# Kernel optimization log

Measured on AMD Instinct MI355X. Metric: run time of the kernel, lower is better.

Reference implementation:

```python
import jax, jax.numpy as jnp
import numpy as np

D_MODEL = 2048
HQ = 32          # query heads
HKV = 8          # kv heads
HD = D_MODEL // HQ   # head_dim = 64
G = HQ // HKV        # group size = 4
THETA = 10000.0


def _rope(x, pos):
    """x: (B, H, T, D), pos: (B, T) int. Rotates even/odd interleaved pairs."""
    D = x.shape[-1]
    inv_freq = THETA ** (-jnp.arange(0, D, 2, dtype=jnp.float32) / D)   # (D/2,)
    ang = pos[:, None, :, None].astype(jnp.float32) * inv_freq          # (B,1,T,D/2)
    cos, sin = jnp.cos(ang), jnp.sin(ang)
    x1, x2 = x[..., 0::2], x[..., 1::2]
    r1 = x1 * cos - x2 * sin
    r2 = x1 * sin + x2 * cos
    return jnp.stack([r1, r2], axis=-1).reshape(x.shape)


def setup_inputs() -> dict:
    key = jax.random.key(0)
    ks = jax.random.split(key, 5)
    B, T = 2, 2048
    s = lambda fan_in: 1.0 / np.sqrt(fan_in)
    return {
        "x": jax.random.normal(ks[0], (B, T, D_MODEL), jnp.float32),
        "token_positions": jnp.arange(T, dtype=jnp.int32),
        "WQ": jax.random.normal(ks[1], (HQ * HD, D_MODEL), jnp.float32) * s(D_MODEL),
        "WK": jax.random.normal(ks[2], (HKV * HD, D_MODEL), jnp.float32) * s(D_MODEL),
        "WV": jax.random.normal(ks[3], (HKV * HD, D_MODEL), jnp.float32) * s(D_MODEL),
        "WO": jax.random.normal(ks[4], (D_MODEL, HQ * HD), jnp.float32) * s(HQ * HD),
    }


def reference(x, token_positions, WQ, WK, WV, WO):
    B, T, _ = x.shape
    pos = token_positions if token_positions.ndim == 2 else jnp.broadcast_to(token_positions[None, :], (B, T))

    # Projections (Linear is y = x @ W.T, no bias)
    Q = (x @ WQ.T).reshape(B, T, HQ, HD).transpose(0, 2, 1, 3)    # (B,Hq,T,D)
    K = (x @ WK.T).reshape(B, T, HKV, HD).transpose(0, 2, 1, 3)   # (B,Hkv,T,D)
    V = (x @ WV.T).reshape(B, T, HKV, HD).transpose(0, 2, 1, 3)

    Q = _rope(Q, pos)
    K = _rope(K, pos)

    # GQA: group query heads per kv head instead of duplicating K/V
    Qg = Q.reshape(B, HKV, G, T, HD)
    scale = jnp.float32(1.0 / np.sqrt(HD))
    scores = jnp.einsum('bkgqd,bkld->bkgql', Qg, K) * scale       # (B,Hkv,G,T,T)

    causal = jnp.tril(jnp.ones((T, T), dtype=bool))
    scores = jnp.where(causal, scores, jnp.finfo(scores.dtype).min)
    A = jax.nn.softmax(scores, axis=-1)

    O = jnp.einsum('bkgql,bkld->bkgqd', A, V)                     # (B,Hkv,G,T,D)
    O = O.reshape(B, HQ, T, HD).transpose(0, 2, 1, 3).reshape(B, T, HQ * HD)
    return O @ WO.T
```

## Files before the change

### kernel.cpp

```cpp
#include <hip/hip_runtime.h>
#include <hip/hip_bf16.h>

#define B_   2
#define T_   2048
#define DM_  2048
#define HQ_  32
#define HKV_ 8
#define HD_  64

typedef __attribute__((ext_vector_type(8))) short bf16x8;
typedef __attribute__((ext_vector_type(4))) float f32x4;
typedef __fp16 f16x4 __attribute__((ext_vector_type(4)));
typedef __fp16 f16x2 __attribute__((ext_vector_type(2)));

__device__ __forceinline__ unsigned short f2bf(float f) {
    unsigned int u = __float_as_uint(f);
    u = (u + 0x7fffu + ((u >> 16) & 1u)) >> 16;
    return (unsigned short)u;
}

__device__ __forceinline__ void gload16(const unsigned short* g, unsigned short* l) {
    __builtin_amdgcn_global_load_lds(
        (const __attribute__((address_space(1))) unsigned int*)g,
        (__attribute__((address_space(3))) unsigned int*)l, 16, 0, 0);
}


#define CONV_N 4718592

__global__ __launch_bounds__(256) void convert_all(
    const float* __restrict__ x,  const float* __restrict__ WQ,
    const float* __restrict__ WK, const float* __restrict__ WV,
    const float* __restrict__ WO, unsigned short* __restrict__ ws,
    const int* __restrict__ pos,  float* __restrict__ trig)
{
    int i = blockIdx.x*256 + threadIdx.x;
    if (i >= CONV_N) {
        int j = i - CONV_N;
        if (j < T_*32) {
            int t = j >> 5, p = j & 31;
            float inv = exp2f(-0.4152410118609203f * (float)p);
            float ang = (float)pos[t] * inv;
            float sn, cs;
            sincosf(ang, &sn, &cs);
            *(float2*)&trig[j*2] = make_float2(cs, sn);
        }
        return;
    }
    const float* src; unsigned short* dst; int rel;
    if (i < 2097152)      { src = x;  dst = ws;                 rel = i; }
    else if (i < 3145728) { src = WQ; dst = ws + 8388608;       rel = i - 2097152; }
    else if (i < 3407872) { src = WK; dst = ws + 8388608+4194304; rel = i - 3145728; }
    else if (i < 3670016) { src = WV; dst = ws + 8388608+5242880; rel = i - 3407872; }
    else                  { src = WO; dst = ws + 14680064;      rel = i - 3670016; }
    float4 v = *(const float4*)(src + (size_t)rel*4);
    uint2 pk;
    pk.x = (unsigned int)f2bf(v.x) | ((unsigned int)f2bf(v.y) << 16);
    pk.y = (unsigned int)f2bf(v.z) | ((unsigned int)f2bf(v.w) << 16);
    *(uint2*)(dst + (size_t)rel*4) = pk;
}

__global__ __launch_bounds__(256) void qkv_gemm_bf16(
    const unsigned short* __restrict__ Ab, const unsigned short* __restrict__ Wb,
    unsigned short* __restrict__ Qb, unsigned short* __restrict__ Kb,
    unsigned short* __restrict__ Vt, const float* __restrict__ trig)
{
    __shared__ unsigned short As[3][128*32];
    __shared__ unsigned short Bs[3][128*32];
    const int tid  = threadIdx.x;
    const int ln   = tid & 63;
    const int wv   = tid >> 6;
    const int wm   = (wv >> 1) * 64;
    const int wn   = (wv & 1) * 64;
    const int col  = ln & 15;
    const int quad = ln >> 4;

    const int bid = blockIdx.x;
    const int swz = (bid & 7) * 96 + (bid >> 3);
    const int n0  = (swz % 24) * 128;
    const int m0  = (swz / 24) * 128;

    const int cg = ((tid & 3) ^ ((tid >> 3) & 3)) * 8;
    const unsigned short* aG = Ab + (size_t)(m0 + (tid>>2))*DM_ + cg;
    const unsigned short* bG = Wb + (size_t)(n0 + (tid>>2))*DM_ + cg;
    const int ck = (quad ^ ((col >> 1) & 3)) * 8;

    f32x4 acc[4][4];
    #pragma unroll
    for (int i=0;i<4;++i)
        #pragma unroll
        for (int j=0;j<4;++j) { acc[i][j][0]=0.f; acc[i][j][1]=0.f; acc[i][j][2]=0.f; acc[i][j][3]=0.f; }

    auto stage = [&](int buf, int k0) {
        unsigned short* aL = &As[buf][wv*512];
        unsigned short* bL = &Bs[buf][wv*512];
        gload16(aG + k0,                  aL);
        gload16(aG + (size_t)64*DM_ + k0, aL + 2048);
        gload16(bG + k0,                  bL);
        gload16(bG + (size_t)64*DM_ + k0, bL + 2048);
    };

    auto kstep = [&](int bc, int k0v, int bstage, bool dostage, bool last) {
        if (last) asm volatile("s_waitcnt vmcnt(0)" ::: "memory");
        else      asm volatile("s_waitcnt vmcnt(4)" ::: "memory");
        __builtin_amdgcn_s_barrier();
        if (dostage) stage(bstage, k0v + 64);
        const unsigned short* Ac = As[bc];
        const unsigned short* Bc = Bs[bc];
        bf16x8 af[4], bfr[4];
        #pragma unroll
        for (int i2=0;i2<4;++i2) {
            af[i2]  = *(const bf16x8*)&Ac[(wm + i2*16 + col)*32 + ck];
            bfr[i2] = *(const bf16x8*)&Bc[(wn + i2*16 + col)*32 + ck];
        }
        #pragma unroll
        for (int i2=0;i2<4;++i2)
            #pragma unroll
            for (int j2=0;j2<4;++j2)
                acc[i2][j2] = __builtin_amdgcn_mfma_f32_16x16x32_bf16(af[i2], bfr[j2], acc[i2][j2], 0, 0, 0);
    };

    stage(0, 0);
    stage(1, 32);

    int k0 = 0;
    for (int rep = 0; rep < 20; ++rep) {
        kstep(0, k0,      2, true, false);
        kstep(1, k0+32,   0, true, false);
        kstep(2, k0+64,   1, true, false);
        k0 += 96;
    }
    kstep(0, 1920, 2, true,  false);
    kstep(1, 1952, 0, true,  false);
    kstep(2, 1984, 1, false, false);
    kstep(0, 2016, 0, false, true);

    const int b  = m0 >> 11;
    const int tb = m0 & 2047;
    #pragma unroll
    for (int j=0;j<4;++j) {
        const int n = n0 + wn + j*16 + col;
        if (n < 2560) {
            const int d   = n & 63;
            const int p   = d >> 1;
            const bool ev = (d & 1) == 0;
            const float sc = (n < 2048) ? 0.18033688011112042f : 1.0f;
            unsigned short* outp = (n < 2048)
                ? Qb + (((size_t)(b*HQ_  + (n>>6)))*T_)*HD_
                : Kb + (((size_t)(b*HKV_ + ((n-2048)>>6)))*T_)*HD_;
            #pragma unroll
            for (int i=0;i<4;++i) {
                const int t0 = tb + wm + i*16 + quad*4;
                #pragma unroll
                for (int r=0;r<4;++r) {
                    float self = acc[i][j][r];
                    float part = __shfl_xor(self, 1);
                    float2 cs  = *(const float2*)&trig[((t0 + r)*32 + p)*2];
                    float out  = ev ? (self*cs.x - part*cs.y)
                                    : (part*cs.y + self*cs.x);
                    out *= sc;
                    unsigned int pk = (unsigned int)f2bf(out);
                    unsigned int po = __shfl_xor(pk, 1);
                    if (ev)
                        *(unsigned int*)(outp + (size_t)(t0 + r)*HD_ + d) = pk | (po << 16);
                }
            }
        } else {
            #pragma unroll
            for (int i=0;i<4;++i) {
                const int t = tb + wm + i*16 + quad*4;
                unsigned short* vp = Vt + (((size_t)(b*HKV_ + ((n-2560)>>6)))*HD_ + (n&63))*T_ + t;
                union { f16x2 h; unsigned int u; } c0, c1;
                c0.h = __builtin_amdgcn_cvt_pkrtz(acc[i][j][0], acc[i][j][1]);
                c1.h = __builtin_amdgcn_cvt_pkrtz(acc[i][j][2], acc[i][j][3]);
                *(unsigned int*)(vp)     = c0.u;
                *(unsigned int*)(vp + 2) = c1.u;
            }
        }
    }
}

__global__ __launch_bounds__(256, 2) void attn_mfma(
    const unsigned short* __restrict__ Qb, const unsigned short* __restrict__ Kb,
    const unsigned short* __restrict__ Vh, unsigned short* __restrict__ Ob)
{
    __shared__ unsigned short Ks[2][64*64];
    __shared__ unsigned short Vs[2][64*64];

    const int tid  = threadIdx.x;
    const int lane = tid & 63;
    const int wave = tid >> 6;
    const int q16  = lane & 15;
    const int quad = lane >> 4;
    const int bxi  = blockIdx.x;
    const int bh   = blockIdx.y;
    const int b    = bh >> 5;
    const int h    = bh & 31;
    const int kvh  = h >> 2;
    const int qa   = bxi;
    const int qbt  = 31 - bxi;
    const int qgA  = qa *64 + wave*16 + q16;
    const int qgB  = qbt*64 + wave*16 + q16;

    const unsigned short* kbase = Kb + ((size_t)(b*HKV_ + kvh))*T_*HD_;
    const unsigned short* vbase = Vh + ((size_t)(b*HKV_ + kvh))*(size_t)HD_*T_;

    const bf16x8 qA0 = *(const bf16x8*)(Qb + ((size_t)bh*T_ + qgA)*HD_ + quad*8);
    const bf16x8 qA1 = *(const bf16x8*)(Qb + ((size_t)bh*T_ + qgA)*HD_ + 32 + quad*8);
    const bf16x8 qB0 = *(const bf16x8*)(Qb + ((size_t)bh*T_ + qgB)*HD_ + quad*8);
    const bf16x8 qB1 = *(const bf16x8*)(Qb + ((size_t)bh*T_ + qgB)*HD_ + 32 + quad*8);

    f32x4 oA[4], oB[4];
    #pragma unroll
    for (int i=0;i<4;++i) {
        oA[i][0]=0.f; oA[i][1]=0.f; oA[i][2]=0.f; oA[i][3]=0.f;
        oB[i][0]=0.f; oB[i][1]=0.f; oB[i][2]=0.f; oB[i][3]=0.f;
    }
    float lA = 0.f, lB = 0.f;

    const int sr = tid >> 3;
    const int sj = tid & 7;
    const int sc = (sj ^ (sr & 7)) * 8;

    const int rk7 = q16 & 7;
    const int ck0 = (quad ^ rk7) * 8;
    const int ck1 = ((quad + 4) ^ rk7) * 8;

    auto smrow = [&](const f32x4 s, float& ps) -> f16x4 {
        float e0 = exp2f(s[0]), e1 = exp2f(s[1]);
        float e2 = exp2f(s[2]), e3 = exp2f(s[3]);
        ps += (e0+e1) + (e2+e3);
        union { f16x2 h[2]; f16x4 v; } c;
        c.h[0] = __builtin_amdgcn_cvt_pkrtz(e0, e1);
        c.h[1] = __builtin_amdgcn_cvt_pkrtz(e2, e3);
        return c.v;
    };

    uint4 kr0, kr1, vr0, vr1;
    kr0 = *(const uint4*)(kbase + (size_t)sr*HD_ + sj*8);
    kr1 = *(const uint4*)(kbase + (size_t)(sr+32)*HD_ + sj*8);
    vr0 = *(const uint4*)(vbase + (size_t)sr*T_ + sj*8);
    vr1 = *(const uint4*)(vbase + (size_t)(sr+32)*T_ + sj*8);
    *(uint4*)&Ks[0][sr*64 + sc]      = kr0;
    *(uint4*)&Ks[0][(sr+32)*64 + sc] = kr1;
    *(uint4*)&Vs[0][sr*64 + sc]      = vr0;
    *(uint4*)&Vs[0][(sr+32)*64 + sc] = vr1;
    kr0 = *(const uint4*)(kbase + (size_t)(64+sr)*HD_ + sj*8);
    kr1 = *(const uint4*)(kbase + (size_t)(64+sr+32)*HD_ + sj*8);
    vr0 = *(const uint4*)(vbase + (size_t)sr*T_ + 64 + sj*8);
    vr1 = *(const uint4*)(vbase + (size_t)(sr+32)*T_ + 64 + sj*8);
    __syncthreads();

    int cur = 0;

    for (int kt = 0; kt <= qa; ++kt) {
        const unsigned short* KsC = Ks[cur];
        const unsigned short* VsC = Vs[cur];
        const int nxt = cur ^ 1;

        f32x4 sB[4], sA[4];
        #pragma unroll
        for (int t=0;t<4;++t) {
            sB[t][0]=0.f; sB[t][1]=0.f; sB[t][2]=0.f; sB[t][3]=0.f;
            sA[t][0]=0.f; sA[t][1]=0.f; sA[t][2]=0.f; sA[t][3]=0.f;
        }
        f16x4 pfB[4];
        float psB = 0.f, psA = 0.f;

        __builtin_amdgcn_s_setprio(1);
        #pragma unroll
        for (int t = 0; t < 4; ++t) {
            const int rk = (t*16 + q16) * 64;
            bf16x8 a0 = *(const bf16x8*)&KsC[rk + ck0];
            bf16x8 a1 = *(const bf16x8*)&KsC[rk + ck1];
            sB[t] = __builtin_amdgcn_mfma_f32_16x16x32_bf16(a0, qB0, sB[t], 0, 0, 0);
            sB[t] = __builtin_amdgcn_mfma_f32_16x16x32_bf16(a1, qB1, sB[t], 0, 0, 0);
            sA[t] = __builtin_amdgcn_mfma_f32_16x16x32_bf16(a0, qA0, sA[t], 0, 0, 0);
            sA[t] = __builtin_amdgcn_mfma_f32_16x16x32_bf16(a1, qA1, sA[t], 0, 0, 0);
            if (t > 0) pfB[t-1] = smrow(sB[t-1], psB);
        }
        *(uint4*)&Ks[nxt][sr*64 + sc]      = kr0;
        *(uint4*)&Ks[nxt][(sr+32)*64 + sc] = kr1;
        *(uint4*)&Vs[nxt][sr*64 + sc]      = vr0;
        *(uint4*)&Vs[nxt][(sr+32)*64 + sc] = vr1;
        if (kt + 1 < qbt) {
            const int kn = (kt+2)*64;
            kr0 = *(const uint4*)(kbase + (size_t)(kn+sr)*HD_ + sj*8);
            kr1 = *(const uint4*)(kbase + (size_t)(kn+sr+32)*HD_ + sj*8);
            vr0 = *(const uint4*)(vbase + (size_t)sr*T_ + kn + sj*8);
            vr1 = *(const uint4*)(vbase + (size_t)(sr+32)*T_ + kn + sj*8);
        }
        pfB[3] = smrow(sB[3], psB);
        lB += psB;

        if (kt == qa) {
            #pragma unroll
            for (int t = 0; t < 4; ++t)
                #pragma unroll
                for (int r = 0; r < 4; ++r)
                    if (kt*64 + t*16 + quad*4 + r > qgA) sA[t][r] = -1e30f;
        }

        #pragma unroll
        for (int t = 0; t < 4; ++t) {
            const int cv = ((2*t + (quad>>1)) ^ rk7) * 8 + (quad&1)*4;
            f16x4 va[4];
            #pragma unroll
            for (int dt=0;dt<4;++dt)
                va[dt] = *(const f16x4*)&VsC[(dt*16 + q16)*64 + cv];
            #pragma unroll
            for (int dt=0;dt<4;++dt)
                oB[dt] = __builtin_amdgcn_mfma_f32_16x16x16f16(va[dt], pfB[t], oB[dt], 0, 0, 0);
            f16x4 pfA = smrow(sA[t], psA);
            #pragma unroll
            for (int dt=0;dt<4;++dt)
                oA[dt] = __builtin_amdgcn_mfma_f32_16x16x16f16(va[dt], pfA, oA[dt], 0, 0, 0);
        }
        lA += psA;
        __builtin_amdgcn_s_setprio(0);
        __syncthreads();
        cur ^= 1;
    }

    for (int kt = qa+1; kt <= qbt; ++kt) {
        const unsigned short* KsC = Ks[cur];
        const unsigned short* VsC = Vs[cur];
        const int nxt = cur ^ 1;

        f32x4 sB[4];
        #pragma unroll
        for (int t=0;t<4;++t) { sB[t][0]=0.f; sB[t][1]=0.f; sB[t][2]=0.f; sB[t][3]=0.f; }

        __builtin_amdgcn_s_setprio(1);
        #pragma unroll
        for (int t = 0; t < 4; ++t) {
            const int rk = (t*16 + q16) * 64;
            bf16x8 a0 = *(const bf16x8*)&KsC[rk + ck0];
            bf16x8 a1 = *(const bf16x8*)&KsC[rk + ck1];
            sB[t] = __builtin_amdgcn_mfma_f32_16x16x32_bf16(a0, qB0, sB[t], 0, 0, 0);
            sB[t] = __builtin_amdgcn_mfma_f32_16x16x32_bf16(a1, qB1, sB[t], 0, 0, 0);
        }
        if (kt < qbt) {
            *(uint4*)&Ks[nxt][sr*64 + sc]      = kr0;
            *(uint4*)&Ks[nxt][(sr+32)*64 + sc] = kr1;
            *(uint4*)&Vs[nxt][sr*64 + sc]      = vr0;
            *(uint4*)&Vs[nxt][(sr+32)*64 + sc] = vr1;
        }
        if (kt + 1 < qbt) {
            const int kn = (kt+2)*64;
            kr0 = *(const uint4*)(kbase + (size_t)(kn+sr)*HD_ + sj*8);
            kr1 = *(const uint4*)(kbase + (size_t)(kn+sr+32)*HD_ + sj*8);
            vr0 = *(const uint4*)(vbase + (size_t)sr*T_ + kn + sj*8);
            vr1 = *(const uint4*)(vbase + (size_t)(sr+32)*T_ + kn + sj*8);
        }
        if (kt == qbt) {
            #pragma unroll
            for (int t = 0; t < 4; ++t)
                #pragma unroll
                for (int r = 0; r < 4; ++r)
                    if (kt*64 + t*16 + quad*4 + r > qgB) sB[t][r] = -1e30f;
        }

        float psB = 0.f;
        #pragma unroll
        for (int t = 0; t < 4; ++t) {
            f16x4 pfB = smrow(sB[t], psB);
            const int cv = ((2*t + (quad>>1)) ^ rk7) * 8 + (quad&1)*4;
            #pragma unroll
            for (int dt=0;dt<4;++dt) {
                f16x4 va = *(const f16x4*)&VsC[(dt*16 + q16)*64 + cv];
                oB[dt] = __builtin_amdgcn_mfma_f32_16x16x16f16(va, pfB, oB[dt], 0, 0, 0);
            }
        }
        lB += psB;
        __builtin_amdgcn_s_setprio(0);
        __syncthreads();
        cur ^= 1;
    }

    lA += __shfl_xor(lA, 16); lA += __shfl_xor(lA, 32);
    lB += __shfl_xor(lB, 16); lB += __shfl_xor(lB, 32);
    const float rlA = 1.0f / lA;
    const float rlB = 1.0f / lB;
    unsigned short* opA = Ob + ((size_t)(b*T_ + qgA))*(HQ_*HD_) + h*HD_;
    unsigned short* opB = Ob + ((size_t)(b*T_ + qgB))*(HQ_*HD_) + h*HD_;
    #pragma unroll
    for (int dt = 0; dt < 4; ++dt) {
        uint2 pa, pb;
        pa.x = (unsigned int)f2bf(oA[dt][0]*rlA) | ((unsigned int)f2bf(oA[dt][1]*rlA) << 16);
        pa.y = (unsigned int)f2bf(oA[dt][2]*rlA) | ((unsigned int)f2bf(oA[dt][3]*rlA) << 16);
        pb.x = (unsigned int)f2bf(oB[dt][0]*rlB) | ((unsigned int)f2bf(oB[dt][1]*rlB) << 16);
        pb.y = (unsigned int)f2bf(oB[dt][2]*rlB) | ((unsigned int)f2bf(oB[dt][3]*rlB) << 16);
        *(uint2*)(opA + dt*16 + quad*4) = pa;
        *(uint2*)(opB + dt*16 + quad*4) = pb;
    }
}

__global__ __launch_bounds__(256) void out_gemm_bf16(
    const unsigned short* __restrict__ Ab, const unsigned short* __restrict__ Wb,
    float* __restrict__ C)
{
    __shared__ unsigned short As[3][128*32];
    __shared__ unsigned short Bs[3][128*32];
    const int tid  = threadIdx.x;
    const int ln   = tid & 63;
    const int wv   = tid >> 6;
    const int wm   = (wv >> 1) * 64;
    const int wn   = (wv & 1) * 64;
    const int col  = ln & 15;
    const int quad = ln >> 4;

    const int bid = blockIdx.x;
    const int swz = (bid & 7) * 64 + (bid >> 3);
    const int n0  = (swz & 15) * 128;
    const int m0  = (swz >> 4) * 128;

    const int cg = ((tid & 3) ^ ((tid >> 3) & 3)) * 8;
    const unsigned short* aG = Ab + (size_t)(m0 + (tid>>2))*DM_ + cg;
    const unsigned short* bG = Wb + (size_t)(n0 + (tid>>2))*DM_ + cg;
    const int ck = (quad ^ ((col >> 1) & 3)) * 8;

    f32x4 acc[4][4];
    #pragma unroll
    for (int i=0;i<4;++i)
        #pragma unroll
        for (int j=0;j<4;++j) { acc[i][j][0]=0.f; acc[i][j][1]=0.f; acc[i][j][2]=0.f; acc[i][j][3]=0.f; }

    auto stage = [&](int buf, int k0) {
        unsigned short* aL = &As[buf][wv*512];
        unsigned short* bL = &Bs[buf][wv*512];
        gload16(aG + k0,                  aL);
        gload16(aG + (size_t)64*DM_ + k0, aL + 2048);
        gload16(bG + k0,                  bL);
        gload16(bG + (size_t)64*DM_ + k0, bL + 2048);
    };

    auto kstep = [&](int bc, int k0v, int bstage, bool dostage, bool last) {
        if (last) asm volatile("s_waitcnt vmcnt(0)" ::: "memory");
        else      asm volatile("s_waitcnt vmcnt(4)" ::: "memory");
        __builtin_amdgcn_s_barrier();
        if (dostage) stage(bstage, k0v + 64);
        const unsigned short* Ac = As[bc];
        const unsigned short* Bc = Bs[bc];
        bf16x8 af[4], bfr[4];
        #pragma unroll
        for (int i2=0;i2<4;++i2) {
            af[i2]  = *(const bf16x8*)&Ac[(wm + i2*16 + col)*32 + ck];
            bfr[i2] = *(const bf16x8*)&Bc[(wn + i2*16 + col)*32 + ck];
        }
        #pragma unroll
        for (int i2=0;i2<4;++i2)
            #pragma unroll
            for (int j2=0;j2<4;++j2)
                acc[i2][j2] = __builtin_amdgcn_mfma_f32_16x16x32_bf16(af[i2], bfr[j2], acc[i2][j2], 0, 0, 0);
    };

    stage(0, 0);
    stage(1, 32);

    int k0 = 0;
    for (int rep = 0; rep < 20; ++rep) {
        kstep(0, k0,      2, true, false);
        kstep(1, k0+32,   0, true, false);
        kstep(2, k0+64,   1, true, false);
        k0 += 96;
    }
    kstep(0, 1920, 2, true,  false);
    kstep(1, 1952, 0, true,  false);
    kstep(2, 1984, 1, false, false);
    kstep(0, 2016, 0, false, true);

    #pragma unroll
    for (int i=0;i<4;++i) {
        const int m = m0 + wm + i*16 + quad*4;
        #pragma unroll
        for (int j=0;j<4;++j) {
            const int n = n0 + wn + j*16 + col;
            #pragma unroll
            for (int r=0;r<4;++r)
                C[(size_t)(m + r)*DM_ + n] = acc[i][j][r];
        }
    }
}

extern "C" void kernel_launch(void* const* d_in, const int* in_sizes, int n_in,
                              void* d_out, int out_size, void* d_ws, size_t ws_size,
                              hipStream_t stream) {
    const float* x   = (const float*)d_in[0];
    const int*   pos = (const int*)  d_in[1];
    const float* WQ  = (const float*)d_in[2];
    const float* WK  = (const float*)d_in[3];
    const float* WV  = (const float*)d_in[4];
    const float* WO  = (const float*)d_in[5];
    float* out = (float*)d_out;

    unsigned short* xb  = (unsigned short*)d_ws;
    unsigned short* Wb  = xb  + (size_t)8388608;
    unsigned short* WOb = Wb  + (size_t)6291456;
    unsigned short* Qb  = WOb + (size_t)4194304;
    unsigned short* Kb  = Qb  + (size_t)8388608;
    unsigned short* Vt  = Kb  + (size_t)2097152;
    unsigned short* Ob  = Vt  + (size_t)2097152;
    float* trig = (float*)Ob;

    convert_all<<<18688, 256, 0, stream>>>(x, WQ, WK, WV, WO, (unsigned short*)d_ws, pos, trig);

    qkv_gemm_bf16<<<768, 256, 0, stream>>>(xb, Wb, Qb, Kb, Vt, trig);

    dim3 g3(16, B_*HQ_);
    attn_mfma<<<g3, 256, 0, stream>>>(Qb, Kb, Vt, Ob);

    out_gemm_bf16<<<512, 256, 0, stream>>>(Ob, WOb, out);
}
```

Baseline: 302.7 us.

## Load GEMM A operand directly into registers, staging only B in LDS

In both the QKV projection and output projection GEMMs, the A tile no longer goes through LDS. Each wave now loads its own A fragments straight from global memory into registers, double-buffered one k-step ahead, and only B keeps the 3-stage LDS pipeline. The vmcnt wait drops from 4 to 2 to match, and the main loop is unrolled to six steps so the two register buffers alternate. This cuts LDS traffic and LDS footprint, but A is now read twice from global (the two waves sharing a row block each fetch it) with strided 64-byte row segments, and register pressure rises.

Measured after the change: 429.3 us. 1.42x slower.

```diff
diff --git a/kernel.cpp b/kernel.cpp
--- a/kernel.cpp
+++ b/kernel.cpp
@@ -60,12 +60,56 @@
     *(uint2*)(dst + (size_t)rel*4) = pk;
 }
 
+#define KSTEP(BC, ARC, ARN, K0V, BS, DOSTAGE, DOLA, LAST)                         \
+  {                                                                               \
+    if (LAST) { asm volatile("s_waitcnt vmcnt(0)" ::: "memory"); }                \
+    else      { asm volatile("s_waitcnt vmcnt(2)" ::: "memory"); }                \
+    __builtin_amdgcn_s_barrier();                                                 \
+    if (DOLA) {                                                                   \
+      _Pragma("unroll")                                                           \
+      for (int i2=0;i2<4;++i2)                                                    \
+        ARN[i2] = *(const bf16x8*)(aR + (size_t)i2*16*DM_ + (K0V) + 32);          \
+    }                                                                             \
+    if (DOSTAGE) stageB(BS, (K0V) + 64);                                          \
+    bf16x8 bfr[4];                                                                \
+    _Pragma("unroll")                                                             \
+    for (int i2=0;i2<4;++i2)                                                      \
+      bfr[i2] = *(const bf16x8*)&Bs[BC][(wn + i2*16 + col)*32 + ck];              \
+    _Pragma("unroll")                                                             \
+    for (int i2=0;i2<4;++i2) {                                                    \
+      _Pragma("unroll")                                                           \
+      for (int j2=0;j2<4;++j2)                                                    \
+        acc[i2][j2] = __builtin_amdgcn_mfma_f32_16x16x32_bf16(ARC[i2], bfr[j2],   \
+                                                              acc[i2][j2], 0,0,0);\
+    }                                                                             \
+  }
+
+#define GEMM_MAIN()                                                               \
+    bf16x8 arP[4], arN[4];                                                        \
+    _Pragma("unroll")                                                             \
+    for (int i=0;i<4;++i) arP[i] = *(const bf16x8*)(aR + (size_t)i*16*DM_);       \
+    stageB(0, 0);                                                                 \
+    stageB(1, 32);                                                                \
+    int k0 = 0;                                                                   \
+    for (int rep=0; rep<10; ++rep) {                               \
+        KSTEP(0, arP, arN, k0,      2, true, true, false);                        \
+        KSTEP(1, arN, arP, k0+32,   0, true, true, false);                        \
+        KSTEP(2, arP, arN, k0+64,   1, true, true, false);                        \
+        KSTEP(0, arN, arP, k0+96,   2, true, true, false);                        \
+        KSTEP(1, arP, arN, k0+128,  0, true, true, false);                        \
+        KSTEP(2, arN, arP, k0+160,  1, true, true, false);                        \
+        k0 += 192;                                                                \
+    }                                                                             \
+    KSTEP(0, arP, arN, 1920, 2, true,  true,  false);             \
+    KSTEP(1, arN, arP, 1952, 0, true,  true,  false);             \
+    KSTEP(2, arP, arN, 1984, 0, false, true,  false);                   \
+    KSTEP(0, arN, arP, 2016, 0, false, false, true);
+
 __global__ __launch_bounds__(256) void qkv_gemm_bf16(
     const unsigned short* __restrict__ Ab, const unsigned short* __restrict__ Wb,
     unsigned short* __restrict__ Qb, unsigned short* __restrict__ Kb,
     unsigned short* __restrict__ Vt, const float* __restrict__ trig)
 {
-    __shared__ unsigned short As[3][128*32];
     __shared__ unsigned short Bs[3][128*32];
     const int tid  = threadIdx.x;
     const int ln   = tid & 63;
@@ -81,9 +125,9 @@
     const int m0  = (swz / 24) * 128;
 
     const int cg = ((tid & 3) ^ ((tid >> 3) & 3)) * 8;
-    const unsigned short* aG = Ab + (size_t)(m0 + (tid>>2))*DM_ + cg;
     const unsigned short* bG = Wb + (size_t)(n0 + (tid>>2))*DM_ + cg;
     const int ck = (quad ^ ((col >> 1) & 3)) * 8;
+    const unsigned short* aR = Ab + (size_t)(m0 + wm + col)*DM_ + quad*8;
 
     f32x4 acc[4][4];
     #pragma unroll
@@ -91,49 +135,13 @@
         #pragma unroll
         for (int j=0;j<4;++j) { acc[i][j][0]=0.f; acc[i][j][1]=0.f; acc[i][j][2]=0.f; acc[i][j][3]=0.f; }
 
-    auto stage = [&](int buf, int k0) {
-        unsigned short* aL = &As[buf][wv*512];
+    auto stageB = [&](int buf, int k0v) {
         unsigned short* bL = &Bs[buf][wv*512];
-        gload16(aG + k0,                  aL);
-        gload16(aG + (size_t)64*DM_ + k0, aL + 2048);
-        gload16(bG + k0,                  bL);
-        gload16(bG + (size_t)64*DM_ + k0, bL + 2048);
+        gload16(bG + k0v,                  bL);
+        gload16(bG + (size_t)64*DM_ + k0v, bL + 2048);
     };
 
-    auto kstep = [&](int bc, int k0v, int bstage, bool dostage, bool last) {
-        if (last) asm volatile("s_waitcnt vmcnt(0)" ::: "memory");
-        else      asm volatile("s_waitcnt vmcnt(4)" ::: "memory");
-        __builtin_amdgcn_s_barrier();
-        if (dostage) stage(bstage, k0v + 64);
-        const unsigned short* Ac = As[bc];
-        const unsigned short* Bc = Bs[bc];
-        bf16x8 af[4], bfr[4];
-        #pragma unroll
-        for (int i2=0;i2<4;++i2) {
-            af[i2]  = *(const bf16x8*)&Ac[(wm + i2*16 + col)*32 + ck];
-            bfr[i2] = *(const bf16x8*)&Bc[(wn + i2*16 + col)*32 + ck];
-        }
-        #pragma unroll
-        for (int i2=0;i2<4;++i2)
-            #pragma unroll
-            for (int j2=0;j2<4;++j2)
-                acc[i2][j2] = __builtin_amdgcn_mfma_f32_16x16x32_bf16(af[i2], bfr[j2], acc[i2][j2], 0, 0, 0);
-    };
-
-    stage(0, 0);
-    stage(1, 32);
-
-    int k0 = 0;
-    for (int rep = 0; rep < 20; ++rep) {
-        kstep(0, k0,      2, true, false);
-        kstep(1, k0+32,   0, true, false);
-        kstep(2, k0+64,   1, true, false);
-        k0 += 96;
-    }
-    kstep(0, 1920, 2, true,  false);
-    kstep(1, 1952, 0, true,  false);
-    kstep(2, 1984, 1, false, false);
-    kstep(0, 2016, 0, false, true);
+    GEMM_MAIN();
 
     const int b  = m0 >> 11;
     const int tb = m0 & 2047;
@@ -400,7 +408,6 @@
     const unsigned short* __restrict__ Ab, const unsigned short* __restrict__ Wb,
     float* __restrict__ C)
 {
-    __shared__ unsigned short As[3][128*32];
     __shared__ unsigned short Bs[3][128*32];
     const int tid  = threadIdx.x;
     const int ln   = tid & 63;
@@ -416,9 +423,9 @@
     const int m0  = (swz >> 4) * 128;
 
     const int cg = ((tid & 3) ^ ((tid >> 3) & 3)) * 8;
-    const unsigned short* aG = Ab + (size_t)(m0 + (tid>>2))*DM_ + cg;
     const unsigned short* bG = Wb + (size_t)(n0 + (tid>>2))*DM_ + cg;
     const int ck = (quad ^ ((col >> 1) & 3)) * 8;
+    const unsigned short* aR = Ab + (size_t)(m0 + wm + col)*DM_ + quad*8;
 
     f32x4 acc[4][4];
     #pragma unroll
@@ -426,49 +433,13 @@
         #pragma unroll
         for (int j=0;j<4;++j) { acc[i][j][0]=0.f; acc[i][j][1]=0.f; acc[i][j][2]=0.f; acc[i][j][3]=0.f; }
 
-    auto stage = [&](int buf, int k0) {
-        unsigned short* aL = &As[buf][wv*512];
+    auto stageB = [&](int buf, int k0v) {
         unsigned short* bL = &Bs[buf][wv*512];
-        gload16(aG + k0,                  aL);
-        gload16(aG + (size_t)64*DM_ + k0, aL + 2048);
-        gload16(bG + k0,                  bL);
-        gload16(bG + (size_t)64*DM_ + k0, bL + 2048);
+        gload16(bG + k0v,                  bL);
+        gload16(bG + (size_t)64*DM_ + k0v, bL + 2048);
     };
 
-    auto kstep = [&](int bc, int k0v, int bstage, bool dostage, bool last) {
-        if (last) asm volatile("s_waitcnt vmcnt(0)" ::: "memory");
-        else      asm volatile("s_waitcnt vmcnt(4)" ::: "memory");
-        __builtin_amdgcn_s_barrier();
-        if (dostage) stage(bstage, k0v + 64);
-        const unsigned short* Ac = As[bc];
-        const unsigned short* Bc = Bs[bc];
-        bf16x8 af[4], bfr[4];
-        #pragma unroll
-        for (int i2=0;i2<4;++i2) {
-            af[i2]  = *(const bf16x8*)&Ac[(wm + i2*16 + col)*32 + ck];
-            bfr[i2] = *(const bf16x8*)&Bc[(wn + i2*16 + col)*32 + ck];
-        }
-        #pragma unroll
-        for (int i2=0;i2<4;++i2)
-            #pragma unroll
-            for (int j2=0;j2<4;++j2)
-                acc[i2][j2] = __builtin_amdgcn_mfma_f32_16x16x32_bf16(af[i2], bfr[j2], acc[i2][j2], 0, 0, 0);
-    };
-
-    stage(0, 0);
-    stage(1, 32);
-
-    int k0 = 0;
-    for (int rep = 0; rep < 20; ++rep) {
-        kstep(0, k0,      2, true, false);
-        kstep(1, k0+32,   0, true, false);
-        kstep(2, k0+64,   1, true, false);
-        k0 += 96;
-    }
-    kstep(0, 1920, 2, true,  false);
-    kstep(1, 1952, 0, true,  false);
-    kstep(2, 1984, 1, false, false);
-    kstep(0, 2016, 0, false, true);
+    GEMM_MAIN();
 
     #pragma unroll
     for (int i=0;i<4;++i) {
```
